# Optimization experiments

Measured on AMD Instinct MI355X. Metric: run time of the kernel, lower is better.

The kernel has to match this reference:

```python
import jax, jax.numpy as jnp
import numpy as np

E = 2048            # total edges in the batch
L = 8               # num_features == max_walk_length
G = 128             # num_graphs in the batch
HID = 128
N_NODES = 4096


def setup_inputs() -> dict:
    key = jax.random.key(0)
    k0, k1, k2, k3 = jax.random.split(key, 4)
    edge_index = jax.random.randint(k0, (2, E), 0, N_NODES, dtype=jnp.int32)
    edge_graph = jnp.sort(jax.random.randint(k1, (E,), 0, G, dtype=jnp.int32))
    W1 = jax.random.normal(k2, (L, HID), dtype=jnp.float32) * (1.0 / np.sqrt(L))
    b1 = jnp.zeros((HID,), dtype=jnp.float32)
    W2 = jax.random.normal(k3, (HID, 1), dtype=jnp.float32) * (1.0 / np.sqrt(HID))
    b2 = jnp.zeros((1,), dtype=jnp.float32)
    return {"edge_index": edge_index, "edge_graph": edge_graph,
            "W1": W1, "b1": b1, "W2": W2, "b2": b2}


def reference(edge_index, edge_graph, W1, b1, W2, b2):
    src, dst = edge_index[0], edge_index[1]  # edge i = (src_i, dst_i)
    # Non-backtracking edge matrix: B[i, j] = 1 iff dst_j == src_i and src_j != dst_i
    # (matches the python condition `u != l and v == k` with edge_i=(k,l), edge_j=(u,v))
    B = ((dst[None, :] == src[:, None]) & (src[None, :] != dst[:, None])).astype(jnp.float32)
    e = B.shape[0]
    walk_len = W1.shape[0]

    # B^1 .. B^L via scan, collecting diagonals (non-backtracking closed-walk counts per edge)
    def step(P, _):
        P = P @ B
        return P, jnp.diagonal(P)

    _, diags = jax.lax.scan(step, jnp.eye(e, dtype=jnp.float32), None, length=walk_len)
    # diags: [L, E] -> per-graph signatures [G, L]
    sig = jax.ops.segment_sum(diags.T, edge_graph, num_segments=G)

    # MLP (eval mode: dropout is identity)
    h = jax.nn.relu(sig @ W1 + b1)
    return h @ W2 + b2
```

## Files before the change

kernel.cpp:

```cpp
#include <hip/hip_runtime.h>


constexpr int E_EDGES  = 2048;
constexpr int L_WALK   = 8;
constexpr int G_GRAPHS = 128;
constexpr int HID      = 128;
constexpr int N_NODES  = 4096;
constexpr int BLOCK    = 1024;
constexpr int CAP      = 2048;

__launch_bounds__(BLOCK, 1)
__global__ void nbc_all(const int* __restrict__ edge_index,
                        const int* __restrict__ edge_graph,
                        const float* __restrict__ W1,
                        const float* __restrict__ b1,
                        const float* __restrict__ W2,
                        const float* __restrict__ b2,
                        float* __restrict__ out)
{
    __shared__ unsigned short s_off[N_NODES + 2];
    __shared__ unsigned long long s_ebucket[E_EDGES];
    __shared__ unsigned char s_graph[E_EDGES];
    __shared__ int s_sig[G_GRAPHS * L_WALK];
    __shared__ unsigned long long s_bufA[CAP];
    __shared__ unsigned long long s_bufB[CAP];
    __shared__ int s_nn[L_WALK + 1];
    __shared__ int s_wavep[16];

    int* s_cnt = (int*)s_bufA;

    const int t    = threadIdx.x;
    const int lane = t & 63;
    const int wave = t >> 6;
    const int* src = edge_index;
    const int* dst = edge_index + E_EDGES;

    for (int n = t; n < N_NODES; n += BLOCK) s_cnt[n] = 0;
    if (t < G_GRAPHS * L_WALK) s_sig[t] = 0;
    if (t <= L_WALK) s_nn[t] = (t == 0) ? E_EDGES : 0;
    __syncthreads();

    for (int e = t; e < E_EDGES; e += BLOCK) {
        atomicAdd(&s_cnt[dst[e]], 1);
        s_graph[e] = (unsigned char)edge_graph[e];
    }
    __syncthreads();

    const int base4 = t * 4;
    int loc[4];
    int run = 0;
    #pragma unroll
    for (int j = 0; j < 4; ++j) { loc[j] = run; run += s_cnt[base4 + j]; }
    int incl = run;
    #pragma unroll
    for (int off = 1; off < 64; off <<= 1) {
        int v = __shfl_up(incl, off);
        if (lane >= off) incl += v;
    }
    if (lane == 63) s_wavep[wave] = incl;
    __syncthreads();
    int wbase = 0;
    for (int w = 0; w < wave; ++w) wbase += s_wavep[w];
    const int start = wbase + incl - run;
    #pragma unroll
    for (int j = 0; j < 4; ++j) s_off[base4 + j] = (unsigned short)(start + loc[j]);
    if (t == 0) s_off[N_NODES] = E_EDGES;
    __syncthreads();

    for (int n = t; n < N_NODES; n += BLOCK) s_cnt[n] = s_off[n];
    __syncthreads();

    for (int e = t; e < E_EDGES; e += BLOCK) {
        int se = src[e], de = dst[e];
        int pos = atomicAdd(&s_cnt[de], 1);
        s_ebucket[pos] = (unsigned long long)e
                       | ((unsigned long long)se << 11)
                       | ((unsigned long long)de << 23)
                       | ((unsigned long long)s_off[se]     << 35)
                       | ((unsigned long long)s_off[se + 1] << 47);
    }
    __syncthreads();

    for (int i = t; i < E_EDGES; i += BLOCK) {
        int se = src[i], de = dst[i];
        s_bufA[i] = (unsigned long long)i
                  | ((unsigned long long)de << 11)
                  | ((unsigned long long)s_off[se]     << 23)
                  | ((unsigned long long)s_off[se + 1] << 35);
    }
    __syncthreads();

    unsigned long long* cur = s_bufA;
    unsigned long long* nxt = s_bufB;
    for (int d = 0; d < L_WALK; ++d) {
        int n_cur = s_nn[d];
        if (n_cur > CAP) n_cur = CAP;
        for (int idx = t; idx < n_cur; idx += BLOCK) {
            unsigned long long e = cur[idx];
            int s   =  e        & 0x7FF;
            int dcc = (e >> 11) & 0xFFF;
            int lo  = (e >> 23) & 0xFFF;
            int hi  = (e >> 35) & 0xFFF;
            for (int p = lo; p < hi; ++p) {
                unsigned long long q = s_ebucket[p];
                int sb = (int)(q >> 11) & 0xFFF;
                if (sb != dcc) {
                    int b = (int)q & 0x7FF;
                    if (b == s) atomicAdd(&s_sig[(int)s_graph[s] * L_WALK + d], 1);
                    if (d < L_WALK - 1) {
                        unsigned long long e2 =
                            (unsigned long long)s | (((q >> 23) & 0xFFFFFFFFFull) << 11);
                        unsigned long long m = __ballot(1);
                        int leader = __ffsll(m) - 1;
                        int rank   = __popcll(m & ((1ull << lane) - 1ull));
                        int bpos = 0;
                        if (lane == leader) bpos = atomicAdd(&s_nn[d + 1], (int)__popcll(m));
                        bpos = __shfl(bpos, leader);
                        int pos = bpos + rank;
                        if (pos < CAP) nxt[pos] = e2;
                    }
                }
            }
        }
        unsigned long long* tmp = cur; cur = nxt; nxt = tmp;
        __syncthreads();
    }

    float* s_part = (float*)s_ebucket;
    {
        const int g   = t >> 3;
        const int sub = t & 7;
        float sig[L_WALK];
        #pragma unroll
        for (int k = 0; k < L_WALK; ++k) sig[k] = (float)s_sig[g * L_WALK + k];
        float o = 0.0f;
        const int j0 = sub * 16;
        #pragma unroll 4
        for (int jj = 0; jj < 16; ++jj) {
            int j = j0 + jj;
            float a = b1[j];
            #pragma unroll
            for (int k = 0; k < L_WALK; ++k) a += sig[k] * W1[k * HID + j];
            o += fmaxf(a, 0.0f) * W2[j];
        }
        s_part[t] = o;
    }
    __syncthreads();
    if (t < G_GRAPHS) {
        float o = b2[0];
        #pragma unroll
        for (int sub = 0; sub < 8; ++sub) o += s_part[t * 8 + sub];
        out[t] = o;
    }
}

extern "C" void kernel_launch(void* const* d_in, const int* in_sizes, int n_in,
                              void* d_out, int out_size, void* d_ws, size_t ws_size,
                              hipStream_t stream) {
    const int*   edge_index = (const int*)d_in[0];
    const int*   edge_graph = (const int*)d_in[1];
    const float* W1 = (const float*)d_in[2];
    const float* b1 = (const float*)d_in[3];
    const float* W2 = (const float*)d_in[4];
    const float* b2 = (const float*)d_in[5];
    float* out = (float*)d_out;

    nbc_all<<<1, BLOCK, 0, stream>>>(edge_index, edge_graph, W1, b1, W2, b2, out);
}
```

Measured before the change: 81.42 us.

## Split single-block kernel into build, multi-block BFS, and MLP kernels

Splits the single-block kernel into three launches. The first builds the edge buckets and the initial frontier in global workspace. The second runs the walk expansion across 32 blocks, each owning a slice of starting edges and copying the bucket table into its own shared memory. The third runs the MLP. This spreads the serial BFS work over many compute units, at the cost of two extra kernel launches, global atomics on the signature counters, and a smaller per-block frontier capacity that could overflow and drop walks.

```diff
diff --git a/kernel.cpp b/kernel.cpp
--- a/kernel.cpp
+++ b/kernel.cpp
@@ -6,28 +6,22 @@
 constexpr int G_GRAPHS = 128;
 constexpr int HID      = 128;
 constexpr int N_NODES  = 4096;
-constexpr int BLOCK    = 1024;
-constexpr int CAP      = 2048;
-
-__launch_bounds__(BLOCK, 1)
-__global__ void nbc_all(const int* __restrict__ edge_index,
-                        const int* __restrict__ edge_graph,
-                        const float* __restrict__ W1,
-                        const float* __restrict__ b1,
-                        const float* __restrict__ W2,
-                        const float* __restrict__ b2,
-                        float* __restrict__ out)
+constexpr int NB_BLOCKS = 32;
+constexpr int SLICE     = E_EDGES / NB_BLOCKS;
+constexpr int CAP       = 1024;
+
+
+
+__launch_bounds__(1024, 1)
+__global__ void k1_build(const int* __restrict__ edge_index,
+                         const int* __restrict__ edge_graph,
+                         unsigned long long* __restrict__ f0,
+                         unsigned long long* __restrict__ ebkt,
+                         int* __restrict__ sig)
 {
-    __shared__ unsigned short s_off[N_NODES + 2];
-    __shared__ unsigned long long s_ebucket[E_EDGES];
-    __shared__ unsigned char s_graph[E_EDGES];
-    __shared__ int s_sig[G_GRAPHS * L_WALK];
-    __shared__ unsigned long long s_bufA[CAP];
-    __shared__ unsigned long long s_bufB[CAP];
-    __shared__ int s_nn[L_WALK + 1];
+    __shared__ int s_cnt[N_NODES];
+    __shared__ unsigned short s_off[N_NODES + 1];
     __shared__ int s_wavep[16];
-
-    int* s_cnt = (int*)s_bufA;
 
     const int t    = threadIdx.x;
     const int lane = t & 63;
@@ -35,15 +29,15 @@
     const int* src = edge_index;
     const int* dst = edge_index + E_EDGES;
 
-    for (int n = t; n < N_NODES; n += BLOCK) s_cnt[n] = 0;
-    if (t < G_GRAPHS * L_WALK) s_sig[t] = 0;
-    if (t <= L_WALK) s_nn[t] = (t == 0) ? E_EDGES : 0;
-    __syncthreads();
-
-    for (int e = t; e < E_EDGES; e += BLOCK) {
-        atomicAdd(&s_cnt[dst[e]], 1);
-        s_graph[e] = (unsigned char)edge_graph[e];
-    }
+    for (int n = t; n < N_NODES; n += 1024) s_cnt[n] = 0;
+    sig[t] = 0;
+    __syncthreads();
+
+    const int se0 = src[t],        de0 = dst[t];
+    const int se1 = src[t + 1024], de1 = dst[t + 1024];
+    const int g0  = edge_graph[t], g1  = edge_graph[t + 1024];
+    atomicAdd(&s_cnt[de0], 1);
+    atomicAdd(&s_cnt[de1], 1);
     __syncthreads();
 
     const int base4 = t * 4;
@@ -64,60 +58,90 @@
     const int start = wbase + incl - run;
     #pragma unroll
     for (int j = 0; j < 4; ++j) s_off[base4 + j] = (unsigned short)(start + loc[j]);
-    if (t == 0) s_off[N_NODES] = E_EDGES;
-    __syncthreads();
-
-    for (int n = t; n < N_NODES; n += BLOCK) s_cnt[n] = s_off[n];
-    __syncthreads();
-
-    for (int e = t; e < E_EDGES; e += BLOCK) {
-        int se = src[e], de = dst[e];
-        int pos = atomicAdd(&s_cnt[de], 1);
-        s_ebucket[pos] = (unsigned long long)e
-                       | ((unsigned long long)se << 11)
-                       | ((unsigned long long)de << 23)
-                       | ((unsigned long long)s_off[se]     << 35)
-                       | ((unsigned long long)s_off[se + 1] << 47);
-    }
-    __syncthreads();
-
-    for (int i = t; i < E_EDGES; i += BLOCK) {
-        int se = src[i], de = dst[i];
-        s_bufA[i] = (unsigned long long)i
-                  | ((unsigned long long)de << 11)
-                  | ((unsigned long long)s_off[se]     << 23)
-                  | ((unsigned long long)s_off[se + 1] << 35);
-    }
-    __syncthreads();
-
-    unsigned long long* cur = s_bufA;
-    unsigned long long* nxt = s_bufB;
+    if (t == 0) s_off[N_NODES] = (unsigned short)E_EDGES;
+    __syncthreads();
+
+    for (int n = t; n < N_NODES; n += 1024) s_cnt[n] = s_off[n];
+    __syncthreads();
+
+    {
+        int p0 = atomicAdd(&s_cnt[de0], 1);
+        ebkt[p0] = (unsigned long long)t
+                 | ((unsigned long long)se0 << 11)
+                 | ((unsigned long long)de0 << 23)
+                 | ((unsigned long long)s_off[se0]     << 35)
+                 | ((unsigned long long)s_off[se0 + 1] << 47);
+        f0[t] = (unsigned long long)t
+              | ((unsigned long long)de0 << 11)
+              | ((unsigned long long)s_off[se0]     << 23)
+              | ((unsigned long long)s_off[se0 + 1] << 35)
+              | ((unsigned long long)g0 << 47);
+    }
+    {
+        int e1 = t + 1024;
+        int p1 = atomicAdd(&s_cnt[de1], 1);
+        ebkt[p1] = (unsigned long long)e1
+                 | ((unsigned long long)se1 << 11)
+                 | ((unsigned long long)de1 << 23)
+                 | ((unsigned long long)s_off[se1]     << 35)
+                 | ((unsigned long long)s_off[se1 + 1] << 47);
+        f0[e1] = (unsigned long long)e1
+               | ((unsigned long long)de1 << 11)
+               | ((unsigned long long)s_off[se1]     << 23)
+               | ((unsigned long long)s_off[se1 + 1] << 35)
+               | ((unsigned long long)g1 << 47);
+    }
+}
+
+__launch_bounds__(256, 1)
+__global__ void k2_bfs(const unsigned long long* __restrict__ f0,
+                       const unsigned long long* __restrict__ ebkt,
+                       int* __restrict__ sig)
+{
+    __shared__ unsigned long long s_eb[E_EDGES];
+    __shared__ unsigned long long bufA[CAP];
+    __shared__ unsigned long long bufB[CAP];
+    __shared__ int s_nn[L_WALK + 1];
+
+    const int t    = threadIdx.x;
+    const int lane = t & 63;
+
+    const ulonglong2* g2 = (const ulonglong2*)ebkt;
+    ulonglong2*       s2 = (ulonglong2*)s_eb;
+    #pragma unroll
+    for (int i = 0; i < 4; ++i) s2[t + 256 * i] = g2[t + 256 * i];
+    if (t < SLICE) bufA[t] = f0[blockIdx.x * SLICE + t];
+    if (t <= L_WALK) s_nn[t] = (t == 0) ? SLICE : 0;
+    __syncthreads();
+
+    unsigned long long* cur = bufA;
+    unsigned long long* nxt = bufB;
     for (int d = 0; d < L_WALK; ++d) {
         int n_cur = s_nn[d];
         if (n_cur > CAP) n_cur = CAP;
-        for (int idx = t; idx < n_cur; idx += BLOCK) {
+        for (int idx = t; idx < n_cur; idx += 256) {
             unsigned long long e = cur[idx];
-            int s   =  e        & 0x7FF;
-            int dcc = (e >> 11) & 0xFFF;
-            int lo  = (e >> 23) & 0xFFF;
-            int hi  = (e >> 35) & 0xFFF;
+            int s   = (int)( e        & 0x7FF);
+            int dcc = (int)((e >> 11) & 0xFFF);
+            int lo  = (int)((e >> 23) & 0xFFF);
+            int hi  = (int)((e >> 35) & 0xFFF);
+            unsigned long long gbits = e & (0x7Full << 47);
             for (int p = lo; p < hi; ++p) {
-                unsigned long long q = s_ebucket[p];
-                int sb = (int)(q >> 11) & 0xFFF;
-                if (sb != dcc) {
-                    int b = (int)q & 0x7FF;
-                    if (b == s) atomicAdd(&s_sig[(int)s_graph[s] * L_WALK + d], 1);
+                unsigned long long q = s_eb[p];
+                if ((int)((q >> 11) & 0xFFF) != dcc) {
+                    int b = (int)(q & 0x7FF);
+                    if (b == s)
+                        atomicAdd(&sig[(int)(gbits >> 47) * L_WALK + d], 1);
                     if (d < L_WALK - 1) {
-                        unsigned long long e2 =
-                            (unsigned long long)s | (((q >> 23) & 0xFFFFFFFFFull) << 11);
+                        unsigned long long e2 = (unsigned long long)s
+                            | (((q >> 23) & 0xFFFFFFFFFull) << 11) | gbits;
                         unsigned long long m = __ballot(1);
                         int leader = __ffsll(m) - 1;
                         int rank   = __popcll(m & ((1ull << lane) - 1ull));
                         int bpos = 0;
                         if (lane == leader) bpos = atomicAdd(&s_nn[d + 1], (int)__popcll(m));
                         bpos = __shfl(bpos, leader);
-                        int pos = bpos + rank;
-                        if (pos < CAP) nxt[pos] = e2;
+                        if (bpos + rank < CAP) nxt[bpos + rank] = e2;
                     }
                 }
             }
@@ -125,32 +149,41 @@
         unsigned long long* tmp = cur; cur = nxt; nxt = tmp;
         __syncthreads();
     }
-
-    float* s_part = (float*)s_ebucket;
-    {
-        const int g   = t >> 3;
-        const int sub = t & 7;
-        float sig[L_WALK];
+}
+
+__launch_bounds__(1024, 1)
+__global__ void k3_mlp(const int* __restrict__ sig,
+                       const float* __restrict__ W1,
+                       const float* __restrict__ b1,
+                       const float* __restrict__ W2,
+                       const float* __restrict__ b2,
+                       float* __restrict__ out)
+{
+    __shared__ float s_part[1024];
+    const int t   = threadIdx.x;
+    const int g   = t >> 3;
+    const int sub = t & 7;
+
+    float sv[L_WALK];
+    #pragma unroll
+    for (int k = 0; k < L_WALK; ++k) sv[k] = (float)sig[g * L_WALK + k];
+    float o = 0.0f;
+    const int j0 = sub * 16;
+    #pragma unroll 4
+    for (int jj = 0; jj < 16; ++jj) {
+        int j = j0 + jj;
+        float a = b1[j];
         #pragma unroll
-        for (int k = 0; k < L_WALK; ++k) sig[k] = (float)s_sig[g * L_WALK + k];
-        float o = 0.0f;
-        const int j0 = sub * 16;
-        #pragma unroll 4
-        for (int jj = 0; jj < 16; ++jj) {
-            int j = j0 + jj;
-            float a = b1[j];
-            #pragma unroll
-            for (int k = 0; k < L_WALK; ++k) a += sig[k] * W1[k * HID + j];
-            o += fmaxf(a, 0.0f) * W2[j];
-        }
-        s_part[t] = o;
-    }
+        for (int k = 0; k < L_WALK; ++k) a += sv[k] * W1[k * HID + j];
+        o += fmaxf(a, 0.0f) * W2[j];
+    }
+    s_part[t] = o;
     __syncthreads();
     if (t < G_GRAPHS) {
-        float o = b2[0];
+        float r = b2[0];
         #pragma unroll
-        for (int sub = 0; sub < 8; ++sub) o += s_part[t * 8 + sub];
-        out[t] = o;
+        for (int s = 0; s < 8; ++s) r += s_part[t * 8 + s];
+        out[t] = r;
     }
 }
 
@@ -165,5 +198,12 @@
     const float* b2 = (const float*)d_in[5];
     float* out = (float*)d_out;
 
-    nbc_all<<<1, BLOCK, 0, stream>>>(edge_index, edge_graph, W1, b1, W2, b2, out);
-}
+    char* ws = (char*)d_ws;
+    unsigned long long* f0   = (unsigned long long*)(ws);
+    unsigned long long* ebkt = (unsigned long long*)(ws + 16384);
+    int*                sig  = (int*)(ws + 32768);
+
+    k1_build<<<1, 1024, 0, stream>>>(edge_index, edge_graph, f0, ebkt, sig);
+    k2_bfs<<<NB_BLOCKS, 256, 0, stream>>>(f0, ebkt, sig);
+    k3_mlp<<<1, 1024, 0, stream>>>(sig, W1, b1, W2, b2, out);
+}
```

Measured after the change: 82.09 us. Within noise of the previous version (+0.8%).

## Replace CSR prefix-scan build with linked-list adjacency via atomicExch

Applied to the files above, without the earlier changes.

Replaces the count/scan/scatter CSR construction over destination nodes with per-node linked lists built by atomicExch on a head array. Each edge node stores its src, dst and next pointer, which removes several block-wide barriers and the prefix-scan phase. The walk expansion now chases list pointers instead of iterating a contiguous range, and the graph id is carried inside the frontier entry. MLP weights are staged into shared memory. Pointer chasing serialises the dependent LDS loads within each walk step, which may cost more than the setup phases it removes.

```diff
diff --git a/kernel.cpp b/kernel.cpp
--- a/kernel.cpp
+++ b/kernel.cpp
@@ -9,6 +9,8 @@
 constexpr int BLOCK    = 1024;
 constexpr int CAP      = 2048;
 
+typedef unsigned long long u64;
+
 __launch_bounds__(BLOCK, 1)
 __global__ void nbc_all(const int* __restrict__ edge_index,
                         const int* __restrict__ edge_graph,
@@ -18,139 +20,111 @@
                         const float* __restrict__ b2,
                         float* __restrict__ out)
 {
-    __shared__ unsigned short s_off[N_NODES + 2];
-    __shared__ unsigned long long s_ebucket[E_EDGES];
-    __shared__ unsigned char s_graph[E_EDGES];
+    __shared__ u64 s_bufA[CAP];
+    __shared__ u64 s_bufB[CAP];
+    __shared__ u64 s_node[E_EDGES];
     __shared__ int s_sig[G_GRAPHS * L_WALK];
-    __shared__ unsigned long long s_bufA[CAP];
-    __shared__ unsigned long long s_bufB[CAP];
     __shared__ int s_nn[L_WALK + 1];
-    __shared__ int s_wavep[16];
+    __shared__ float s_W1[L_WALK * HID];
+    __shared__ float s_b1[HID];
+    __shared__ float s_W2[HID];
+    __shared__ float s_b2;
 
-    int* s_cnt = (int*)s_bufA;
+    int* s_head = (int*)s_bufA;
 
     const int t    = threadIdx.x;
     const int lane = t & 63;
-    const int wave = t >> 6;
-    const int* src = edge_index;
-    const int* dst = edge_index + E_EDGES;
 
-    for (int n = t; n < N_NODES; n += BLOCK) s_cnt[n] = 0;
-    if (t < G_GRAPHS * L_WALK) s_sig[t] = 0;
+    const int2 se2 = ((const int2*)edge_index)[t];
+    const int2 de2 = ((const int2*)(edge_index + E_EDGES))[t];
+    const int2 ge2 = ((const int2*)edge_graph)[t];
+    s_W1[t] = W1[t];
+    if (t < HID) { s_b1[t] = b1[t]; s_W2[t] = W2[t]; }
+    if (t == 0) s_b2 = b2[0];
+    s_sig[t] = 0;
     if (t <= L_WALK) s_nn[t] = (t == 0) ? E_EDGES : 0;
+    for (int n = t; n < N_NODES; n += BLOCK) s_head[n] = -1;
     __syncthreads();
 
-    for (int e = t; e < E_EDGES; e += BLOCK) {
-        atomicAdd(&s_cnt[dst[e]], 1);
-        s_graph[e] = (unsigned char)edge_graph[e];
+    const int e0 = 2 * t, e1 = 2 * t + 1;
+    {
+        int prev0 = atomicExch(&s_head[de2.x], e0);
+        s_node[e0] = (u64)se2.x | ((u64)de2.x << 12) | ((u64)(prev0 & 0xFFF) << 36);
+        int prev1 = atomicExch(&s_head[de2.y], e1);
+        s_node[e1] = (u64)se2.y | ((u64)de2.y << 12) | ((u64)(prev1 & 0xFFF) << 36);
     }
     __syncthreads();
 
-    const int base4 = t * 4;
-    int loc[4];
-    int run = 0;
-    #pragma unroll
-    for (int j = 0; j < 4; ++j) { loc[j] = run; run += s_cnt[base4 + j]; }
-    int incl = run;
-    #pragma unroll
-    for (int off = 1; off < 64; off <<= 1) {
-        int v = __shfl_up(incl, off);
-        if (lane >= off) incl += v;
-    }
-    if (lane == 63) s_wavep[wave] = incl;
+    const int h0 = s_head[se2.x] & 0xFFF;
+    const int h1 = s_head[se2.y] & 0xFFF;
+    s_node[e0] |= (u64)h0 << 24;
+    s_node[e1] |= (u64)h1 << 24;
     __syncthreads();
-    int wbase = 0;
-    for (int w = 0; w < wave; ++w) wbase += s_wavep[w];
-    const int start = wbase + incl - run;
-    #pragma unroll
-    for (int j = 0; j < 4; ++j) s_off[base4 + j] = (unsigned short)(start + loc[j]);
-    if (t == 0) s_off[N_NODES] = E_EDGES;
+    s_bufA[e0] = (u64)e0 | ((u64)de2.x << 11) | ((u64)h0 << 23) | ((u64)ge2.x << 35);
+    s_bufA[e1] = (u64)e1 | ((u64)de2.y << 11) | ((u64)h1 << 23) | ((u64)ge2.y << 35);
     __syncthreads();
 
-    for (int n = t; n < N_NODES; n += BLOCK) s_cnt[n] = s_off[n];
-    __syncthreads();
-
-    for (int e = t; e < E_EDGES; e += BLOCK) {
-        int se = src[e], de = dst[e];
-        int pos = atomicAdd(&s_cnt[de], 1);
-        s_ebucket[pos] = (unsigned long long)e
-                       | ((unsigned long long)se << 11)
-                       | ((unsigned long long)de << 23)
-                       | ((unsigned long long)s_off[se]     << 35)
-                       | ((unsigned long long)s_off[se + 1] << 47);
-    }
-    __syncthreads();
-
-    for (int i = t; i < E_EDGES; i += BLOCK) {
-        int se = src[i], de = dst[i];
-        s_bufA[i] = (unsigned long long)i
-                  | ((unsigned long long)de << 11)
-                  | ((unsigned long long)s_off[se]     << 23)
-                  | ((unsigned long long)s_off[se + 1] << 35);
-    }
-    __syncthreads();
-
-    unsigned long long* cur = s_bufA;
-    unsigned long long* nxt = s_bufB;
+    u64* cur = s_bufA;
+    u64* nxt = s_bufB;
     for (int d = 0; d < L_WALK; ++d) {
         int n_cur = s_nn[d];
         if (n_cur > CAP) n_cur = CAP;
         for (int idx = t; idx < n_cur; idx += BLOCK) {
-            unsigned long long e = cur[idx];
-            int s   =  e        & 0x7FF;
-            int dcc = (e >> 11) & 0xFFF;
-            int lo  = (e >> 23) & 0xFFF;
-            int hi  = (e >> 35) & 0xFFF;
-            for (int p = lo; p < hi; ++p) {
-                unsigned long long q = s_ebucket[p];
-                int sb = (int)(q >> 11) & 0xFFF;
+            u64 e = cur[idx];
+            int s   = (int)( e        & 0x7FF);
+            int dcc = (int)((e >> 11) & 0xFFF);
+            int ptr = (int)((e >> 23) & 0xFFF);
+            u64 gb  = e & (0x7Full << 35);
+            while (ptr != 0xFFF) {
+                u64 q = s_node[ptr];
+                int sb = (int)(q & 0xFFF);
+                int nx = (int)((q >> 36) & 0xFFF);
                 if (sb != dcc) {
-                    int b = (int)q & 0x7FF;
-                    if (b == s) atomicAdd(&s_sig[(int)s_graph[s] * L_WALK + d], 1);
+                    if (ptr == s)
+                        atomicAdd(&s_sig[(int)(gb >> 35) * L_WALK + d], 1);
                     if (d < L_WALK - 1) {
-                        unsigned long long e2 =
-                            (unsigned long long)s | (((q >> 23) & 0xFFFFFFFFFull) << 11);
-                        unsigned long long m = __ballot(1);
+                        u64 e2 = (u64)s | (((q >> 12) & 0xFFFFFFull) << 11) | gb;
+                        u64 m = __ballot(1);
                         int leader = __ffsll(m) - 1;
                         int rank   = __popcll(m & ((1ull << lane) - 1ull));
                         int bpos = 0;
                         if (lane == leader) bpos = atomicAdd(&s_nn[d + 1], (int)__popcll(m));
                         bpos = __shfl(bpos, leader);
-                        int pos = bpos + rank;
-                        if (pos < CAP) nxt[pos] = e2;
+                        if (bpos + rank < CAP) nxt[bpos + rank] = e2;
                     }
                 }
+                ptr = nx;
             }
         }
-        unsigned long long* tmp = cur; cur = nxt; nxt = tmp;
+        u64* tmp = cur; cur = nxt; nxt = tmp;
         __syncthreads();
     }
 
-    float* s_part = (float*)s_ebucket;
+    float* s_part = (float*)s_node;
     {
         const int g   = t >> 3;
         const int sub = t & 7;
-        float sig[L_WALK];
+        float sv[L_WALK];
         #pragma unroll
-        for (int k = 0; k < L_WALK; ++k) sig[k] = (float)s_sig[g * L_WALK + k];
+        for (int k = 0; k < L_WALK; ++k) sv[k] = (float)s_sig[g * L_WALK + k];
         float o = 0.0f;
         const int j0 = sub * 16;
         #pragma unroll 4
         for (int jj = 0; jj < 16; ++jj) {
             int j = j0 + jj;
-            float a = b1[j];
+            float a = s_b1[j];
             #pragma unroll
-            for (int k = 0; k < L_WALK; ++k) a += sig[k] * W1[k * HID + j];
-            o += fmaxf(a, 0.0f) * W2[j];
+            for (int k = 0; k < L_WALK; ++k) a += sv[k] * s_W1[k * HID + j];
+            o += fmaxf(a, 0.0f) * s_W2[j];
         }
         s_part[t] = o;
     }
     __syncthreads();
     if (t < G_GRAPHS) {
-        float o = b2[0];
+        float r = s_b2;
         #pragma unroll
-        for (int sub = 0; sub < 8; ++sub) o += s_part[t * 8 + sub];
-        out[t] = o;
+        for (int s = 0; s < 8; ++s) r += s_part[t * 8 + s];
+        out[t] = r;
     }
 }
 
```

After: 73.75 us. 1.1x faster.
